# Performance work log

Measured on AMD Instinct MI355X. Metric: run time of the kernel, lower is better.

## Reference

```python
import jax, jax.numpy as jnp
import numpy as np

SEQ, B, V, E, H, L = 64, 64, 32000, 512, 512, 2


def setup_inputs() -> dict:
    key = jax.random.key(0)
    ks = jax.random.split(key, 12)
    k = float(np.sqrt(1.0 / H))
    u = lambda kk, shape, a, b: jax.random.uniform(kk, shape, jnp.float32, a, b)
    return {
        "inputs": jax.random.randint(ks[0], (SEQ, B), 0, V),          # [T, B] token ids
        "hidden": jnp.zeros((L, B, H), jnp.float32),                   # initial hidden
        "emb": u(ks[1], (V, E), -0.1, 0.1),                            # embedding table
        "Wr_w": u(ks[2], (L, H, E + H), -k, k),                        # reset gate [L,H,2H]
        "Wr_b": u(ks[3], (L, H), -k, k),
        "Wz_w": u(ks[4], (L, H, E + H), -k, k),                        # update gate
        "Wz_b": u(ks[5], (L, H), -k, k),
        "Wh_w": u(ks[6], (L, H, E + H), -k, k),                        # candidate
        "Wh_b": u(ks[7], (L, H), -k, k),
        "out_w": u(ks[8], (V, H), -0.1, 0.1),                          # output projection
        "out_b": jnp.zeros((V,), jnp.float32),
    }


def reference(inputs, hidden, emb, Wr_w, Wr_b, Wz_w, Wz_b, Wh_w, Wh_b, out_w, out_b):
    # GRU recurrence over time via lax.scan (dropout disabled: dp_keep_prob=1.0)
    def step(h, tok):
        x = emb[tok]  # [B, E]
        new_h = []
        for i in range(L):  # fixed small layer loop
            hi = h[i]  # [B, H]
            cat = jnp.concatenate([x, hi], axis=1)  # [B, E+H]
            r = jax.nn.sigmoid(cat @ Wr_w[i].T + Wr_b[i])
            z = jax.nn.sigmoid(cat @ Wz_w[i].T + Wz_b[i])
            h_hat = jnp.tanh(jnp.concatenate([x, r * hi], axis=1) @ Wh_w[i].T + Wh_b[i])
            x = (1.0 - z) * hi + z * h_hat  # next layer input / new hidden
            new_h.append(x)
        logits_t = x @ out_w.T + out_b  # [B, V]
        return jnp.stack(new_h), logits_t

    hidden_final, logits = jax.lax.scan(step, hidden, inputs)
    return logits, hidden_final  # [T,B,V], [L,B,H]
```

## Files before the change

### kernel.cpp

```cpp
#include <hip/hip_runtime.h>

constexpr int NT = 64;
constexpr int NB = 64;
constexpr int NV = 32000;
constexpr int NE = 512;
constexpr int NH = 512;
constexpr int NPAIR = 16 * 250;

constexpr size_t SZ_OW  = (size_t)NV * NE;
constexpr size_t SZ_XE  = (size_t)NT * NB * NE;
constexpr size_t SZ_H   = (size_t)NB * NH;
constexpr size_t LOGITS = (size_t)NT * NB * NV;

typedef float f32x4 __attribute__((ext_vector_type(4)));
typedef int   i32x4 __attribute__((ext_vector_type(4)));
typedef short bf16x8 __attribute__((ext_vector_type(8)));
typedef short s16x4 __attribute__((ext_vector_type(4)));
typedef _Float16 f16x8 __attribute__((ext_vector_type(8)));

__device__ __forceinline__ unsigned short f2bf(float x) {
  unsigned u = __float_as_uint(x);
  u += 0x7FFFu + ((u >> 16) & 1u);
  return (unsigned short)(u >> 16);
}
__device__ __forceinline__ float bf2f(unsigned short s) {
  return __uint_as_float(((unsigned)s) << 16);
}
__device__ __forceinline__ void split2(float v, short* hi, short* lo) {
  unsigned short h = f2bf(v);
  *hi = (short)h;
  *lo = (short)f2bf(v - bf2f(h));
}
__device__ __forceinline__ f32x4 mma_bf16(bf16x8 a, bf16x8 b, f32x4 c) {
  return __builtin_amdgcn_mfma_f32_16x16x32_bf16(a, b, c, 0, 0, 0);
}
__device__ __forceinline__ f32x4 mma_f16(f16x8 a, f16x8 b, f32x4 c) {
  return __builtin_amdgcn_mfma_f32_16x16x32_f16(a, b, c, 0, 0, 0);
}
__device__ __forceinline__ float fast_sigmoid(float x) {
  return __builtin_amdgcn_rcpf(1.0f + __expf(-x));
}
__device__ __forceinline__ float fast_tanh(float x) {
  return 1.0f - 2.0f * __builtin_amdgcn_rcpf(1.0f + __expf(2.0f * x));
}

__device__ __forceinline__ void st_sc32u(unsigned* p, unsigned v) {
  asm volatile("global_store_dword %0, %1, off sc0 sc1" :: "v"(p), "v"(v) : "memory");
}
__device__ __forceinline__ void st_sc128(void* p, i32x4 v) {
  asm volatile("global_store_dwordx4 %0, %1, off sc0 sc1" :: "v"(p), "v"(v) : "memory");
}
__device__ __forceinline__ void st_nt(float* p, float v) {
  asm volatile("global_store_dword %0, %1, off nt" :: "v"(p), "v"(v) : "memory");
}
__device__ __forceinline__ unsigned ld_sc32u(const unsigned* p) {
  unsigned v;
  asm volatile("global_load_dword %0, %1, off sc0 sc1\n\ts_waitcnt vmcnt(0)"
               : "=v"(v) : "v"(p) : "memory");
  return v;
}

__device__ __forceinline__ void wait1(const unsigned* flags, int slot, unsigned thr) {
  while (ld_sc32u(&flags[(size_t)slot * 32]) < thr) {}
}
__device__ __forceinline__ void wave_poll4(const unsigned* flags, int slotBase, int cgBase,
                                           int rh, unsigned thr, int lane) {
  const unsigned* fp = &flags[(size_t)(slotBase + (cgBase + (lane & 3)) * 2 + rh) * 32];
  while (!__all((int)(ld_sc32u(fp) >= thr))) {}
}
__device__ __forceinline__ void wave_poll8(const unsigned* flags, int slotBase, int cgBase,
                                           int rh, unsigned thr, int lane) {
  const unsigned* fp = &flags[(size_t)(slotBase + (cgBase + (lane & 7)) * 2 + rh) * 32];
  while (!__all((int)(ld_sc32u(fp) >= thr))) {}
}

__device__ __forceinline__ void publish(unsigned* flags, int slot, unsigned val) {
  asm volatile("s_waitcnt vmcnt(0)" ::: "memory");
  __syncthreads();
  if (threadIdx.x == 0) st_sc32u(&flags[(size_t)slot * 32], val);
}

__global__ void k_prep(
    const float* __restrict__ outw, const int* __restrict__ toks,
    const float* __restrict__ emb, const float* __restrict__ hid,
    _Float16* OWf, short* XeHi, short* XeLo,
    short* X1Hi, short* X1Lo, short* h0Hi, short* h0Lo) {
  const size_t stride = (size_t)gridDim.x * blockDim.x;
  const size_t N1 = SZ_OW, N2 = N1 + SZ_XE, N3 = N2 + SZ_H, N4 = N3 + SZ_H;
  for (size_t x = (size_t)blockIdx.x * blockDim.x + threadIdx.x; x < N4; x += stride) {
    if (x < N1) {
      OWf[x] = (_Float16)outw[x];
    } else if (x < N2) {
      size_t p = x - N1;
      size_t r = p >> 9, c = p & 511u;
      int tok = toks[r];
      float v = emb[(size_t)tok * 512 + c];
      short hi, lo; split2(v, &hi, &lo);
      XeHi[p] = hi; XeLo[p] = lo;
    } else if (x < N3) {
      size_t p = x - N2;
      short hi, lo; split2(hid[p], &hi, &lo);
      h0Hi[p] = hi; h0Lo[p] = lo;
    } else {
      size_t p = x - N3;
      short hi, lo; split2(hid[SZ_H + p], &hi, &lo);
      X1Hi[p] = hi; X1Lo[p] = lo;
    }
  }
}

__device__ __forceinline__ void mmaP32(
    const short* __restrict__ aH, const short* __restrict__ aL, int base,
    const short* lsHi_, const short* lsLo_,
    f32x4 (&accH)[2], f32x4 (&accL)[2], int wave, int l15, int lq) {
  const int kq = wave >> 1, rhalf = wave & 1;
  const int r0 = rhalf * 16 + l15;
#pragma unroll
  for (int i = 0; i < 4; ++i) {
    const int ko = kq * 128 + i * 32 + lq * 8;
    const int kg = base + ko;
    const int e0 = (l15 * 1024 + kg) ^ ((l15 & 7) << 3);
    const int e1 = ((16 + l15) * 1024 + kg) ^ ((l15 & 7) << 3);
    bf16x8 bh0 = *(const bf16x8*)&lsHi_[e0];
    bf16x8 bl0 = *(const bf16x8*)&lsLo_[e0];
    bf16x8 bh1 = *(const bf16x8*)&lsHi_[e1];
    bf16x8 bl1 = *(const bf16x8*)&lsLo_[e1];
    bf16x8 ah = *(const bf16x8*)&aH[r0 * 512 + ko];
    bf16x8 al = *(const bf16x8*)&aL[r0 * 512 + ko];
    accH[0] = mma_bf16(ah, bh0, accH[0]);
    accH[1] = mma_bf16(ah, bh1, accH[1]);
    accL[0] = mma_bf16(al, bh0, accL[0]);
    accL[1] = mma_bf16(al, bh1, accL[1]);
    accL[0] = mma_bf16(ah, bl0, accL[0]);
    accL[1] = mma_bf16(ah, bl1, accL[1]);
  }
}
__device__ __forceinline__ void reduce4(float* lsRed_, f32x4 (&accH)[2], f32x4 (&accL)[2],
                                        f32x4 (&acc)[2], int wave, int l15, int lq) {
  const int kq = wave >> 1, rhalf = wave & 1;
  acc[0] = accH[0] + accL[0];
  acc[1] = accH[1] + accL[1];
  const int pos = l15 * 16 + lq * 4;
  if (kq) {
    *(f32x4*)&lsRed_[(((kq - 1) * 2 + rhalf) * 2 + 0) * 256 + pos] = acc[0];
    *(f32x4*)&lsRed_[(((kq - 1) * 2 + rhalf) * 2 + 1) * 256 + pos] = acc[1];
  }
  __syncthreads();
  if (!kq) {
#pragma unroll
    for (int s = 0; s < 3; ++s) {
      acc[0] += *(const f32x4*)&lsRed_[((s * 2 + rhalf) * 2 + 0) * 256 + pos];
      acc[1] += *(const f32x4*)&lsRed_[((s * 2 + rhalf) * 2 + 1) * 256 + pos];
    }
  }
  __syncthreads();
}

__device__ __forceinline__ void mmaD(
    const short* __restrict__ pAH, const short* __restrict__ pAL,
    int kloc0, int kkGlob0, const short* lsHi_, const short* lsLo_,
    f32x4 (&accH)[2], f32x4 (&accL)[2], int l15, int lq, int rhalf, int rowbase) {
  const int r0 = rowbase + rhalf * 16 + l15;
#pragma unroll 4
  for (int i = 0; i < 8; ++i) {
    const int kk = kkGlob0 + i * 32 + lq * 8;
    const int ka = kloc0 + i * 32 + lq * 8;
    const int e0 = (l15 * 1024 + kk) ^ ((l15 & 7) << 3);
    const int e1 = ((16 + l15) * 1024 + kk) ^ ((l15 & 7) << 3);
    bf16x8 bh0 = *(const bf16x8*)&lsHi_[e0];
    bf16x8 bl0 = *(const bf16x8*)&lsLo_[e0];
    bf16x8 bh1 = *(const bf16x8*)&lsHi_[e1];
    bf16x8 bl1 = *(const bf16x8*)&lsLo_[e1];
    bf16x8 ah = *(const bf16x8*)&pAH[r0 * 512 + ka];
    bf16x8 al = *(const bf16x8*)&pAL[r0 * 512 + ka];
    accH[0] = mma_bf16(ah, bh0, accH[0]);
    accH[1] = mma_bf16(ah, bh1, accH[1]);
    accL[0] = mma_bf16(al, bh0, accL[0]);
    accL[1] = mma_bf16(al, bh1, accL[1]);
    accL[0] = mma_bf16(ah, bl0, accL[0]);
    accL[1] = mma_bf16(ah, bl1, accL[1]);
  }
}
__device__ __forceinline__ void reduceD(float* lsRed_, f32x4 (&accH)[2], f32x4 (&accL)[2],
                                        f32x4 (&acc)[2], int wave, int l15, int lq) {
  acc[0] = accH[0] + accL[0];
  acc[1] = accH[1] + accL[1];
  const int pos = l15 * 16 + lq * 4;
  if (wave >= 2) {
    *(f32x4*)&lsRed_[((wave - 2) * 2 + 0) * 256 + pos] = acc[0];
    *(f32x4*)&lsRed_[((wave - 2) * 2 + 1) * 256 + pos] = acc[1];
  }
  __syncthreads();
  if (wave < 2) {
#pragma unroll
    for (int s = 0; s < 3; ++s) {
      const int slot = (wave & 1) + 2 * s;
      acc[0] += *(const f32x4*)&lsRed_[(slot * 2 + 0) * 256 + pos];
      acc[1] += *(const f32x4*)&lsRed_[(slot * 2 + 1) * 256 + pos];
    }
  }
  __syncthreads();
}

__device__ __forceinline__ void stage_weights(
    short* lsHi, short* lsLo, const float* srcBase0, const float* srcBase1,
    int jc, int tid) {
  for (int i = tid; i < 8192; i += 512) {
    const int j = i >> 8;
    const int k4 = (i & 255) << 2;
    const int g = jc + j;
    const float* src = (srcBase1 && g >= 512)
        ? (srcBase1 + (size_t)(g - 512) * 1024 + k4)
        : (srcBase0 + (size_t)g * 1024 + k4);
    f32x4 v = *(const f32x4*)src;
    s16x4 h4, l4;
#pragma unroll
    for (int q = 0; q < 4; ++q) { short hi, lo; split2(v[q], &hi, &lo); h4[q] = hi; l4[q] = lo; }
    const int els = (j * 1024 + k4) ^ ((j & 7) << 3);
    *(s16x4*)&lsHi[els] = h4;
    *(s16x4*)&lsLo[els] = l4;
  }
}

__device__ void gemm_loop(char* pool, int tid,
                          const _Float16* Af, const _Float16* Bw,
                          const float* bias, float* C,
                          unsigned* flags, unsigned* tcnt) {
  _Float16* lsA0 = (_Float16*)pool;
  _Float16* lsA1 = lsA0 + 128 * 64;
  _Float16* lsB  = lsA1 + 128 * 64;
  volatile int* bc = (volatile int*)(pool + 49152);
  const int wave = tid >> 6, lane = tid & 63, l15 = lane & 15, lq = lane >> 4;
  const int wr = (wave >> 2) * 64, wc = (wave & 3) * 32;
  unsigned lastR = 0;
  __syncthreads();
  for (;;) {
    if (tid == 0)
      *bc = (int)__hip_atomic_fetch_add(tcnt, 1u, __ATOMIC_RELAXED,
                                        __HIP_MEMORY_SCOPE_AGENT);
    __syncthreads();
    const int pr = *bc;
    __syncthreads();
    if (pr >= NPAIR) break;
    const int p = pr / 250, bn = pr - p * 250;
    const unsigned Rneed = 4u * (unsigned)p + 4u;
    if (lastR < Rneed) {
      if (tid < 32) {
        const unsigned* fp = &flags[(size_t)(160 + tid) * 32];
        while (ld_sc32u(fp) < Rneed) __builtin_amdgcn_s_sleep(8);
      }
      lastR = Rneed;
    }
    __syncthreads();
    f32x4 acc0[4][2] = {}, acc1[4][2] = {};
    const size_t arow0 = (size_t)p * 256;
    const size_t brow0 = (size_t)bn * 128;
    for (int kb = 0; kb < 512; kb += 64) {
#pragma unroll
      for (int i = 0; i < 2; ++i) {
        int c = tid + i * 512;
        int row = c >> 3, kc = (c & 7) * 8;
        int el = (row * 64 + kc) ^ ((row & 7) << 3);
        *(f16x8*)&lsA0[el] = *(const f16x8*)(Af + (arow0 + row) * 512 + kb + kc);
        *(f16x8*)&lsA1[el] = *(const f16x8*)(Af + (arow0 + 128 + row) * 512 + kb + kc);
        *(f16x8*)&lsB[el]  = *(const f16x8*)(Bw + (brow0 + row) * 512 + kb + kc);
      }
      __syncthreads();
#pragma unroll
      for (int k0 = 0; k0 < 64; k0 += 32) {
        const int kk = k0 + lq * 8;
        f16x8 af0[4], af1[4], bfr[2];
#pragma unroll
        for (int i = 0; i < 4; ++i) {
          int ra = wr + i * 16 + l15;
          int el = (ra * 64 + kk) ^ ((ra & 7) << 3);
          af0[i] = *(const f16x8*)&lsA0[el];
          af1[i] = *(const f16x8*)&lsA1[el];
        }
#pragma unroll
        for (int jt = 0; jt < 2; ++jt) {
          int rb = wc + jt * 16 + l15;
          bfr[jt] = *(const f16x8*)&lsB[(rb * 64 + kk) ^ ((rb & 7) << 3)];
        }
#pragma unroll
        for (int i = 0; i < 4; ++i)
#pragma unroll
          for (int jt = 0; jt < 2; ++jt) {
            acc0[i][jt] = mma_f16(af0[i], bfr[jt], acc0[i][jt]);
            acc1[i][jt] = mma_f16(af1[i], bfr[jt], acc1[i][jt]);
          }
      }
      __syncthreads();
    }
    const float b0v = bias[brow0 + wc + l15];
    const float b1v = bias[brow0 + wc + 16 + l15];
#pragma unroll
    for (int i = 0; i < 4; ++i) {
#pragma unroll
      for (int r = 0; r < 4; ++r) {
        const size_t row = arow0 + wr + i * 16 + lq * 4 + r;
        float* pa = C + row * (size_t)NV + brow0 + wc + l15;
        st_nt(pa, acc0[i][0][r] + b0v);
        st_nt(pa + 16, acc0[i][1][r] + b1v);
        float* pb = pa + (size_t)128 * NV;
        st_nt(pb, acc1[i][0][r] + b0v);
        st_nt(pb + 16, acc1[i][1][r] + b1v);
      }
    }
  }
}

__launch_bounds__(512, 1)
__global__ void k_main(
    const float* __restrict__ Wr, const float* __restrict__ Wz, const float* __restrict__ Wh,
    const float* __restrict__ Wrb, const float* __restrict__ Wzb, const float* __restrict__ Whb,
    const short* __restrict__ XeHi, const short* __restrict__ XeLo,
    short* X1Hi, short* X1Lo, _Float16* X1f16,
    short* h0Hi, short* h0Lo,
    short* rh0Hi, short* rh0Lo, short* rh1Hi, short* rh1Lo,
    float* z0, float* z1, float* hidOut,
    const _Float16* OWf, const float* outb, float* out,
    unsigned* flags, unsigned* tcnt) {
  __shared__ __align__(16) char pool[153600];
  short* lsHi = (short*)pool;
  short* lsLo = lsHi + 32 * 1024;
  float* lsRed = (float*)(pool + 131072);
  short* sH    = (short*)(pool + 131072);
  short* sL    = sH + 1024;
  float* sZA   = (float*)(pool + 131072);
  short* stH   = (short*)(pool + 143360);
  short* stL   = stH + 1024;
  float* sZ    = (float*)(pool + 147456);
  _Float16* sX = (_Float16*)(pool + 151552);

  const int wg = blockIdx.x;
  const int tid = threadIdx.x;
  const int wave = tid >> 6, lane = tid & 63, l15 = lane & 15, lq = lane >> 4;

  if (wg < 64) {
    const int cg = wg >> 1, rh = wg & 1, jc = cg * 32, rowbase = rh * 32;
    const bool isR = (jc < 512);
    stage_weights(lsHi, lsLo, Wr, Wz, jc, tid);
    float biasL0, biasL1;
    {
      const int j0 = jc + l15, j1 = j0 + 16;
      biasL0 = (j0 < 512) ? Wrb[j0] : Wzb[j0 - 512];
      biasL1 = (j1 < 512) ? Wrb[j1] : Wzb[j1 - 512];
    }
    __syncthreads();
    for (int t = 0; t < NT; ++t) {
      f32x4 accH[2] = {}, accL[2] = {};
      mmaP32(XeHi + (size_t)t * SZ_H + rowbase * 512,
             XeLo + (size_t)t * SZ_H + rowbase * 512, 0,
             lsHi, lsLo, accH, accL, wave, l15, lq);
      const short* hH = h0Hi + (size_t)t * SZ_H + rowbase * 512;
      const short* hL = h0Lo + (size_t)t * SZ_H + rowbase * 512;
      i32x4 pre;
      const int pbuf = tid >> 7, pq = tid & 127, prow = pq >> 2, pc = pq & 3;
      if (isR && tid < 256) {
        wait1(flags, 128 + ((jc >> 5) * 2 + rh), (unsigned)t);
        pre = *(const i32x4*)((pbuf ? hL : hH) + prow * 512 + jc + pc * 8);
      }
      wave_poll4(flags, 128, 4 * (wave >> 1), rh, (unsigned)t, lane);
      mmaP32(hH, hL, 512, lsHi, lsLo, accH, accL, wave, l15, lq);
      if (isR && tid < 256)
        *(i32x4*)&(pbuf ? stL : stH)[prow * 32 + pc * 8] = pre;
      f32x4 acc[2];
      reduce4(lsRed, accH, accL, acc, wave, l15, lq);
      if (wave < 2) {
#pragma unroll
        for (int ct = 0; ct < 2; ++ct) {
          const int jj = ct * 16 + l15;
          const float bv = ct ? biasL1 : biasL0;
#pragma unroll
          for (int r = 0; r < 4; ++r) {
            const int lb = wave * 16 + lq * 4 + r;
            const float s = fast_sigmoid(acc[ct][r] + bv);
            if (isR) {
              const float hv = bf2f((unsigned short)stH[lb * 32 + jj]) +
                               bf2f((unsigned short)stL[lb * 32 + jj]);
              short hi, lo; split2(s * hv, &hi, &lo);
              sH[lb * 32 + jj] = hi; sL[lb * 32 + jj] = lo;
            } else {
              sZA[lb * 32 + jj] = s;
            }
          }
        }
      }
      __syncthreads();
      if (isR) {
        if (tid < 256) {
          i32x4 v = *(const i32x4*)&(pbuf ? sL : sH)[prow * 32 + pc * 8];
          st_sc128((pbuf ? rh0Lo : rh0Hi) + (size_t)t * SZ_H +
                   (size_t)(rowbase + prow) * 512 + jc + pc * 8, v);
        }
      } else {
        if (tid < 256) {
          const int row = tid >> 3, c = tid & 7;
          i32x4 v = *(const i32x4*)&sZA[row * 32 + c * 4];
          st_sc128(z0 + (size_t)t * SZ_H + (size_t)(rowbase + row) * 512 +
                   (jc - 512) + c * 4, v);
        }
      }
      publish(flags, wg, (unsigned)(t + 1));
    }
  } else if (wg < 128) {
    const int idx = wg - 64, cg = idx >> 1, rh = idx & 1, jc = cg * 32, rowbase = rh * 32;
    const bool isR = (jc < 512);
    stage_weights(lsHi, lsLo, Wr + (size_t)512 * 1024, Wz + (size_t)512 * 1024, jc, tid);
    float biasL0, biasL1;
    {
      const int j0 = jc + l15, j1 = j0 + 16;
      biasL0 = (j0 < 512) ? Wrb[512 + j0] : Wzb[512 + j0 - 512];
      biasL1 = (j1 < 512) ? Wrb[512 + j1] : Wzb[512 + j1 - 512];
    }
    __syncthreads();
    for (int t = 0; t < NT; ++t) {
      const short* xH = h0Hi + (size_t)(t + 1) * SZ_H;
      const short* xL = h0Lo + (size_t)(t + 1) * SZ_H;
      const short* hH = X1Hi + (size_t)t * SZ_H;
      const short* hL = X1Lo + (size_t)t * SZ_H;
      i32x4 pre;
      const int pbuf = tid >> 7, pq = tid & 127, prow = pq >> 2, pc = pq & 3;
      if (isR && tid < 256) {
        wait1(flags, 160 + ((jc >> 5) * 2 + rh), (unsigned)t);
        pre = *(const i32x4*)((pbuf ? hL : hH) +
                              (size_t)(rowbase + prow) * 512 + jc + pc * 8);
      }
      f32x4 accH[2] = {}, accL[2] = {};
      {
        const int khalf = wave >> 1, rhalf = wave & 1;
        if (khalf < 2) wave_poll8(flags, 128, (khalf & 1) * 8, rh, (unsigned)(t + 1), lane);
        else           wave_poll8(flags, 160, (khalf & 1) * 8, rh, (unsigned)t, lane);
        const short* pAH = (khalf < 2) ? xH : hH;
        const short* pAL = (khalf < 2) ? xL : hL;
        mmaD(pAH, pAL, (khalf & 1) * 256, khalf * 256, lsHi, lsLo,
             accH, accL, l15, lq, rhalf, rowbase);
      }
      if (isR && tid < 256)
        *(i32x4*)&(pbuf ? stL : stH)[prow * 32 + pc * 8] = pre;
      f32x4 acc[2];
      reduceD(lsRed, accH, accL, acc, wave, l15, lq);
      if (wave < 2) {
#pragma unroll
        for (int ct = 0; ct < 2; ++ct) {
          const int jj = ct * 16 + l15;
          const float bv = ct ? biasL1 : biasL0;
#pragma unroll
          for (int r = 0; r < 4; ++r) {
            const int lb = wave * 16 + lq * 4 + r;
            const float s = fast_sigmoid(acc[ct][r] + bv);
            if (isR) {
              const float hv = bf2f((unsigned short)stH[lb * 32 + jj]) +
                               bf2f((unsigned short)stL[lb * 32 + jj]);
              short hi, lo; split2(s * hv, &hi, &lo);
              sH[lb * 32 + jj] = hi; sL[lb * 32 + jj] = lo;
            } else {
              sZA[lb * 32 + jj] = s;
            }
          }
        }
      }
      __syncthreads();
      if (isR) {
        if (tid < 256) {
          i32x4 v = *(const i32x4*)&(pbuf ? sL : sH)[prow * 32 + pc * 8];
          st_sc128((pbuf ? rh1Lo : rh1Hi) + (size_t)t * SZ_H +
                   (size_t)(rowbase + prow) * 512 + jc + pc * 8, v);
        }
      } else {
        if (tid < 256) {
          const int row = tid >> 3, c = tid & 7;
          i32x4 v = *(const i32x4*)&sZA[row * 32 + c * 4];
          st_sc128(z1 + (size_t)t * SZ_H + (size_t)(rowbase + row) * 512 +
                   (jc - 512) + c * 4, v);
        }
      }
      publish(flags, wg, (unsigned)(t + 1));
    }
  } else if (wg < 192) {
    const bool isL1 = (wg >= 160);
    const int idx = isL1 ? (wg - 160) : (wg - 128);
    const int cg = idx >> 1, rh = idx & 1, jc = cg * 32, rowbase = rh * 32;
    const int layer = isL1 ? 1 : 0;
    stage_weights(lsHi, lsLo, Wh + (size_t)layer * 512 * 1024, nullptr, jc, tid);
    const float biasL0 = Whb[layer * 512 + jc + l15];
    const float biasL1 = Whb[layer * 512 + jc + 16 + l15];
    __syncthreads();
    short* myHi = isL1 ? X1Hi : h0Hi;
    short* myLo = isL1 ? X1Lo : h0Lo;
    const short* rhHi_ = isL1 ? rh1Hi : rh0Hi;
    const short* rhLo_ = isL1 ? rh1Lo : rh0Lo;
    const float* zArr = isL1 ? z1 : z0;
    const int fbase = isL1 ? 64 : 0;
    for (int t = 0; t < NT; ++t) {
      const int pbuf = tid >> 7, pq = tid & 127, prow = pq >> 2, pc = pq & 3;
      if (tid < 256) {
        const short* src = (pbuf ? myLo : myHi) + (size_t)t * SZ_H +
                           (size_t)(rowbase + prow) * 512 + jc + pc * 8;
        *(i32x4*)&(pbuf ? stL : stH)[prow * 32 + pc * 8] = *(const i32x4*)src;
      }
      f32x4 accH[2] = {}, accL[2] = {};
      if (isL1) {
        wave_poll4(flags, 128, 4 * (wave >> 1), rh, (unsigned)(t + 1), lane);
        mmaP32(h0Hi + (size_t)(t + 1) * SZ_H + rowbase * 512,
               h0Lo + (size_t)(t + 1) * SZ_H + rowbase * 512, 0,
               lsHi, lsLo, accH, accL, wave, l15, lq);
      } else {
        mmaP32(XeHi + (size_t)t * SZ_H + rowbase * 512,
               XeLo + (size_t)t * SZ_H + rowbase * 512, 0,
               lsHi, lsLo, accH, accL, wave, l15, lq);
      }
      f32x4 zv;
      const int zrow = tid >> 3, zc = tid & 7;
      if (tid < 256) {
        wait1(flags, fbase + ((16 + (jc >> 5)) * 2 + rh), (unsigned)(t + 1));
        zv = *(const f32x4*)(zArr + (size_t)t * SZ_H +
                             (size_t)(rowbase + zrow) * 512 + jc + zc * 4);
      }
      wave_poll4(flags, fbase, 4 * (wave >> 1), rh, (unsigned)(t + 1), lane);
      mmaP32(rhHi_ + (size_t)t * SZ_H + rowbase * 512,
             rhLo_ + (size_t)t * SZ_H + rowbase * 512, 512,
             lsHi, lsLo, accH, accL, wave, l15, lq);
      if (tid < 256)
        *(f32x4*)&sZ[zrow * 32 + zc * 4] = zv;
      f32x4 acc[2];
      reduce4(lsRed, accH, accL, acc, wave, l15, lq);
      if (wave < 2) {
#pragma unroll
        for (int ct = 0; ct < 2; ++ct) {
          const int jj = ct * 16 + l15, j = jc + jj;
          const float bv = ct ? biasL1 : biasL0;
#pragma unroll
          for (int r = 0; r < 4; ++r) {
            const int lb = wave * 16 + lq * 4 + r;
            const float hh = fast_tanh(acc[ct][r] + bv);
            const float z = sZ[lb * 32 + jj];
            const float ho = bf2f((unsigned short)stH[lb * 32 + jj]) +
                             bf2f((unsigned short)stL[lb * 32 + jj]);
            const float hn = (1.0f - z) * ho + z * hh;
            short hi, lo; split2(hn, &hi, &lo);
            sH[lb * 32 + jj] = hi; sL[lb * 32 + jj] = lo;
            if (isL1) sX[lb * 32 + jj] = (_Float16)hn;
            if (t == NT - 1)
              hidOut[(size_t)layer * SZ_H + (size_t)(rowbase + lb) * 512 + j] = hn;
          }
        }
      }
      __syncthreads();
      if (tid < 256) {
        i32x4 v = *(const i32x4*)&(pbuf ? sL : sH)[prow * 32 + pc * 8];
        st_sc128((pbuf ? myLo : myHi) + (size_t)(t + 1) * SZ_H +
                 (size_t)(rowbase + prow) * 512 + jc + pc * 8, v);
      } else if (isL1 && tid < 384) {
        const int q = tid - 256, row = q >> 2, c = q & 3;
        i32x4 v = *(const i32x4*)&sX[row * 32 + c * 8];
        st_sc128(X1f16 + (size_t)t * SZ_H + (size_t)(rowbase + row) * 512 + jc + c * 8, v);
      }
      publish(flags, wg, (unsigned)(t + 1));
    }
  }
  gemm_loop(pool, tid, X1f16, OWf, outb, out, flags, tcnt);
}

extern "C" void kernel_launch(void* const* d_in, const int* in_sizes, int n_in,
                              void* d_out, int out_size, void* d_ws, size_t ws_size,
                              hipStream_t stream) {
  (void)in_sizes; (void)n_in; (void)out_size; (void)ws_size;
  const int*   toks = (const int*)d_in[0];
  const float* hid  = (const float*)d_in[1];
  const float* emb  = (const float*)d_in[2];
  const float* Wr   = (const float*)d_in[3];
  const float* Wrb  = (const float*)d_in[4];
  const float* Wz   = (const float*)d_in[5];
  const float* Wzb  = (const float*)d_in[6];
  const float* Wh   = (const float*)d_in[7];
  const float* Whb  = (const float*)d_in[8];
  const float* outw = (const float*)d_in[9];
  const float* outb = (const float*)d_in[10];
  float* out = (float*)d_out;

  char* base = (char*)d_ws;
  size_t off = 0;
  auto carve = [&](size_t bytes) -> char* {
    char* r = base + off;
    off = (off + bytes + 255) & ~(size_t)255;
    return r;
  };
  _Float16* OWf   = (_Float16*)carve(SZ_OW * 2);
  short*    XeHi  = (short*)carve(SZ_XE * 2);
  short*    XeLo  = (short*)carve(SZ_XE * 2);
  short*    X1Hi  = (short*)carve((size_t)(NT + 1) * SZ_H * 2);
  short*    X1Lo  = (short*)carve((size_t)(NT + 1) * SZ_H * 2);
  _Float16* X1f16 = (_Float16*)carve((size_t)NT * SZ_H * 2);
  short*    h0Hi  = (short*)carve((size_t)(NT + 1) * SZ_H * 2);
  short*    h0Lo  = (short*)carve((size_t)(NT + 1) * SZ_H * 2);
  short*    rh0Hi = (short*)carve((size_t)NT * SZ_H * 2);
  short*    rh0Lo = (short*)carve((size_t)NT * SZ_H * 2);
  short*    rh1Hi = (short*)carve((size_t)NT * SZ_H * 2);
  short*    rh1Lo = (short*)carve((size_t)NT * SZ_H * 2);
  float*    z0    = (float*)carve((size_t)NT * SZ_H * 4);
  float*    z1    = (float*)carve((size_t)NT * SZ_H * 4);
  unsigned* flags = (unsigned*)carve(32768);
  unsigned* tcnt  = (unsigned*)carve(256);

  hipMemsetAsync(flags, 0, 32768, stream);
  hipMemsetAsync(tcnt, 0, 256, stream);

  k_prep<<<2048, 256, 0, stream>>>(outw, toks, emb, hid,
                                   OWf, XeHi, XeLo, X1Hi, X1Lo, h0Hi, h0Lo);

  k_main<<<256, 512, 0, stream>>>(
      Wr, Wz, Wh, Wrb, Wzb, Whb, XeHi, XeLo,
      X1Hi, X1Lo, X1f16, h0Hi, h0Lo,
      rh0Hi, rh0Lo, rh1Hi, rh1Lo, z0, z1,
      out + LOGITS, OWf, outb, out, flags, tcnt);
}
```

Baseline: 698.4 us.

## Switch GRU recurrence to per-wave tiles with wave-level flags and no block barriers

Reorganizes the persistent recurrent workgroups so each wave computes a full 16x16 output tile over the whole K range, removing cross-wave LDS reductions and __syncthreads. Synchronization moves from per-workgroup flags to per-wave flags, so consumers poll only the specific producer tiles they need. The recurrent workgroup count drops from 192 to 96 (each handles all 64 batch rows), and the hidden state stays in registers instead of being reloaded. The aim is a shorter serial critical path per timestep, at the cost of more flag polling traffic and more K-work per wave.

Result: slower. 1.668 ms (+138.8%).

```diff
diff --git a/kernel.cpp b/kernel.cpp
--- a/kernel.cpp
+++ b/kernel.cpp
@@ -60,24 +60,12 @@
   return v;
 }
 
-__device__ __forceinline__ void wait1(const unsigned* flags, int slot, unsigned thr) {
-  while (ld_sc32u(&flags[(size_t)slot * 32]) < thr) {}
-}
-__device__ __forceinline__ void wave_poll4(const unsigned* flags, int slotBase, int cgBase,
-                                           int rh, unsigned thr, int lane) {
-  const unsigned* fp = &flags[(size_t)(slotBase + (cgBase + (lane & 3)) * 2 + rh) * 32];
+__device__ __forceinline__ void wave_poll(const unsigned* fp, unsigned thr) {
   while (!__all((int)(ld_sc32u(fp) >= thr))) {}
 }
-__device__ __forceinline__ void wave_poll8(const unsigned* flags, int slotBase, int cgBase,
-                                           int rh, unsigned thr, int lane) {
-  const unsigned* fp = &flags[(size_t)(slotBase + (cgBase + (lane & 7)) * 2 + rh) * 32];
-  while (!__all((int)(ld_sc32u(fp) >= thr))) {}
-}
-
-__device__ __forceinline__ void publish(unsigned* flags, int slot, unsigned val) {
+__device__ __forceinline__ void wpublish(unsigned* flags, int slot, unsigned val, int lane) {
   asm volatile("s_waitcnt vmcnt(0)" ::: "memory");
-  __syncthreads();
-  if (threadIdx.x == 0) st_sc32u(&flags[(size_t)slot * 32], val);
+  if (lane == 0) st_sc32u(&flags[(size_t)slot * 32], val);
 }
 
 __global__ void k_prep(
@@ -109,97 +97,31 @@
   }
 }
 
-__device__ __forceinline__ void mmaP32(
-    const short* __restrict__ aH, const short* __restrict__ aL, int base,
-    const short* lsHi_, const short* lsLo_,
-    f32x4 (&accH)[2], f32x4 (&accL)[2], int wave, int l15, int lq) {
-  const int kq = wave >> 1, rhalf = wave & 1;
-  const int r0 = rhalf * 16 + l15;
-#pragma unroll
-  for (int i = 0; i < 4; ++i) {
-    const int ko = kq * 128 + i * 32 + lq * 8;
-    const int kg = base + ko;
-    const int e0 = (l15 * 1024 + kg) ^ ((l15 & 7) << 3);
-    const int e1 = ((16 + l15) * 1024 + kg) ^ ((l15 & 7) << 3);
-    bf16x8 bh0 = *(const bf16x8*)&lsHi_[e0];
-    bf16x8 bl0 = *(const bf16x8*)&lsLo_[e0];
-    bf16x8 bh1 = *(const bf16x8*)&lsHi_[e1];
-    bf16x8 bl1 = *(const bf16x8*)&lsLo_[e1];
-    bf16x8 ah = *(const bf16x8*)&aH[r0 * 512 + ko];
-    bf16x8 al = *(const bf16x8*)&aL[r0 * 512 + ko];
-    accH[0] = mma_bf16(ah, bh0, accH[0]);
-    accH[1] = mma_bf16(ah, bh1, accH[1]);
-    accL[0] = mma_bf16(al, bh0, accL[0]);
-    accL[1] = mma_bf16(al, bh1, accL[1]);
-    accL[0] = mma_bf16(ah, bl0, accL[0]);
-    accL[1] = mma_bf16(ah, bl1, accL[1]);
+__device__ __forceinline__ void waveMMA16(
+    const short* __restrict__ aH, const short* __restrict__ aL,
+    int r0, int wkb, const short* lsHi_, const short* lsLo_, int wrow,
+    f32x4 (&accH)[2], f32x4 (&accL)[2], int lq) {
+#pragma unroll
+  for (int blk = 0; blk < 16; blk += 8) {
+    bf16x8 ah[8], al[8];
+#pragma unroll
+    for (int i = 0; i < 8; ++i) {
+      const int ka = (blk + i) * 32 + lq * 8;
+      ah[i] = *(const bf16x8*)&aH[r0 * 512 + ka];
+      al[i] = *(const bf16x8*)&aL[r0 * 512 + ka];
+    }
+#pragma unroll
+    for (int i = 0; i < 8; ++i) {
+      const int kg = wkb + (blk + i) * 32 + lq * 8;
+      const int e = (wrow * 1024 + kg) ^ ((wrow & 7) << 3);
+      bf16x8 bh = *(const bf16x8*)&lsHi_[e];
+      bf16x8 bl = *(const bf16x8*)&lsLo_[e];
+      const int p = i & 1;
+      accH[p] = mma_bf16(ah[i], bh, accH[p]);
+      accL[p] = mma_bf16(al[i], bh, accL[p]);
+      accL[p] = mma_bf16(ah[i], bl, accL[p]);
+    }
   }
-}
-__device__ __forceinline__ void reduce4(float* lsRed_, f32x4 (&accH)[2], f32x4 (&accL)[2],
-                                        f32x4 (&acc)[2], int wave, int l15, int lq) {
-  const int kq = wave >> 1, rhalf = wave & 1;
-  acc[0] = accH[0] + accL[0];
-  acc[1] = accH[1] + accL[1];
-  const int pos = l15 * 16 + lq * 4;
-  if (kq) {
-    *(f32x4*)&lsRed_[(((kq - 1) * 2 + rhalf) * 2 + 0) * 256 + pos] = acc[0];
-    *(f32x4*)&lsRed_[(((kq - 1) * 2 + rhalf) * 2 + 1) * 256 + pos] = acc[1];
-  }
-  __syncthreads();
-  if (!kq) {
-#pragma unroll
-    for (int s = 0; s < 3; ++s) {
-      acc[0] += *(const f32x4*)&lsRed_[((s * 2 + rhalf) * 2 + 0) * 256 + pos];
-      acc[1] += *(const f32x4*)&lsRed_[((s * 2 + rhalf) * 2 + 1) * 256 + pos];
-    }
-  }
-  __syncthreads();
-}
-
-__device__ __forceinline__ void mmaD(
-    const short* __restrict__ pAH, const short* __restrict__ pAL,
-    int kloc0, int kkGlob0, const short* lsHi_, const short* lsLo_,
-    f32x4 (&accH)[2], f32x4 (&accL)[2], int l15, int lq, int rhalf, int rowbase) {
-  const int r0 = rowbase + rhalf * 16 + l15;
-#pragma unroll 4
-  for (int i = 0; i < 8; ++i) {
-    const int kk = kkGlob0 + i * 32 + lq * 8;
-    const int ka = kloc0 + i * 32 + lq * 8;
-    const int e0 = (l15 * 1024 + kk) ^ ((l15 & 7) << 3);
-    const int e1 = ((16 + l15) * 1024 + kk) ^ ((l15 & 7) << 3);
-    bf16x8 bh0 = *(const bf16x8*)&lsHi_[e0];
-    bf16x8 bl0 = *(const bf16x8*)&lsLo_[e0];
-    bf16x8 bh1 = *(const bf16x8*)&lsHi_[e1];
-    bf16x8 bl1 = *(const bf16x8*)&lsLo_[e1];
-    bf16x8 ah = *(const bf16x8*)&pAH[r0 * 512 + ka];
-    bf16x8 al = *(const bf16x8*)&pAL[r0 * 512 + ka];
-    accH[0] = mma_bf16(ah, bh0, accH[0]);
-    accH[1] = mma_bf16(ah, bh1, accH[1]);
-    accL[0] = mma_bf16(al, bh0, accL[0]);
-    accL[1] = mma_bf16(al, bh1, accL[1]);
-    accL[0] = mma_bf16(ah, bl0, accL[0]);
-    accL[1] = mma_bf16(ah, bl1, accL[1]);
-  }
-}
-__device__ __forceinline__ void reduceD(float* lsRed_, f32x4 (&accH)[2], f32x4 (&accL)[2],
-                                        f32x4 (&acc)[2], int wave, int l15, int lq) {
-  acc[0] = accH[0] + accL[0];
-  acc[1] = accH[1] + accL[1];
-  const int pos = l15 * 16 + lq * 4;
-  if (wave >= 2) {
-    *(f32x4*)&lsRed_[((wave - 2) * 2 + 0) * 256 + pos] = acc[0];
-    *(f32x4*)&lsRed_[((wave - 2) * 2 + 1) * 256 + pos] = acc[1];
-  }
-  __syncthreads();
-  if (wave < 2) {
-#pragma unroll
-    for (int s = 0; s < 3; ++s) {
-      const int slot = (wave & 1) + 2 * s;
-      acc[0] += *(const f32x4*)&lsRed_[(slot * 2 + 0) * 256 + pos];
-      acc[1] += *(const f32x4*)&lsRed_[(slot * 2 + 1) * 256 + pos];
-    }
-  }
-  __syncthreads();
 }
 
 __device__ __forceinline__ void stage_weights(
@@ -220,6 +142,18 @@
     *(s16x4*)&lsHi[els] = h4;
     *(s16x4*)&lsLo[els] = l4;
   }
+}
+
+__device__ __forceinline__ void wave_store16(
+    const short* scrH, const short* scrL,
+    short* gHi, short* gLo, int rt, int colBase, int lane) {
+  asm volatile("s_waitcnt lgkmcnt(0)" ::: "memory");
+  const int rr = lane >> 2, cc = lane & 3;
+  i32x4 v;
+  if (cc < 2) v = *(const i32x4*)&scrH[rr * 16 + cc * 8];
+  else        v = *(const i32x4*)&scrL[rr * 16 + (cc - 2) * 8];
+  short* dst = (cc < 2 ? gHi : gLo) + (size_t)(rt * 16 + rr) * 512 + colBase + (cc & 1) * 8;
+  st_sc128(dst, v);
 }
 
 __device__ void gemm_loop(char* pool, int tid,
@@ -245,9 +179,13 @@
     const int p = pr / 250, bn = pr - p * 250;
     const unsigned Rneed = 4u * (unsigned)p + 4u;
     if (lastR < Rneed) {
-      if (tid < 32) {
-        const unsigned* fp = &flags[(size_t)(160 + tid) * 32];
-        while (ld_sc32u(fp) < Rneed) __builtin_amdgcn_s_sleep(8);
+      {
+        const unsigned* fp = &flags[(size_t)((80 + (lane >> 3)) * 8 + (lane & 7)) * 32];
+        while (!__all((int)(ld_sc32u(fp) >= Rneed))) __builtin_amdgcn_s_sleep(8);
+      }
+      {
+        const unsigned* fp = &flags[(size_t)((88 + (lane >> 3)) * 8 + (lane & 7)) * 32];
+        while (!__all((int)(ld_sc32u(fp) >= Rneed))) __builtin_amdgcn_s_sleep(8);
       }
       lastR = Rneed;
     }
@@ -314,6 +252,7 @@
 __global__ void k_main(
     const float* __restrict__ Wr, const float* __restrict__ Wz, const float* __restrict__ Wh,
     const float* __restrict__ Wrb, const float* __restrict__ Wzb, const float* __restrict__ Whb,
+    const float* __restrict__ hid,
     const short* __restrict__ XeHi, const short* __restrict__ XeLo,
     short* X1Hi, short* X1Lo, _Float16* X1f16,
     short* h0Hi, short* h0Lo,
@@ -321,243 +260,194 @@
     float* z0, float* z1, float* hidOut,
     const _Float16* OWf, const float* outb, float* out,
     unsigned* flags, unsigned* tcnt) {
-  __shared__ __align__(16) char pool[153600];
+  __shared__ __align__(16) char pool[147456];
   short* lsHi = (short*)pool;
   short* lsLo = lsHi + 32 * 1024;
-  float* lsRed = (float*)(pool + 131072);
-  short* sH    = (short*)(pool + 131072);
-  short* sL    = sH + 1024;
-  float* sZA   = (float*)(pool + 131072);
-  short* stH   = (short*)(pool + 143360);
-  short* stL   = stH + 1024;
-  float* sZ    = (float*)(pool + 147456);
-  _Float16* sX = (_Float16*)(pool + 151552);
+  char* wscrBase = pool + 131072;
 
   const int wg = blockIdx.x;
   const int tid = threadIdx.x;
   const int wave = tid >> 6, lane = tid & 63, l15 = lane & 15, lq = lane >> 4;
+  const int ct = wave >> 2, rt = wave & 3;
+  const int r0 = rt * 16 + l15;
+  short* scrH = (short*)(wscrBase + wave * 2048);
+  short* scrL = scrH + 256;
+  _Float16* scrX = (_Float16*)(scrH + 512);
+  float* scrF = (float*)scrH;
 
   if (wg < 64) {
-    const int cg = wg >> 1, rh = wg & 1, jc = cg * 32, rowbase = rh * 32;
-    const bool isR = (jc < 512);
-    stage_weights(lsHi, lsLo, Wr, Wz, jc, tid);
-    float biasL0, biasL1;
+    const bool isL1 = (wg >= 32);
+    const int cg = isL1 ? (wg - 32) : wg;
+    const int jc = cg * 32;
+    const bool isR = (cg < 16);
+    const int wrow = ct * 16 + l15;
+    stage_weights(lsHi, lsLo, Wr + (isL1 ? (size_t)512 * 1024 : 0),
+                  Wz + (isL1 ? (size_t)512 * 1024 : 0), jc, tid);
+    float bv;
     {
-      const int j0 = jc + l15, j1 = j0 + 16;
-      biasL0 = (j0 < 512) ? Wrb[j0] : Wzb[j0 - 512];
-      biasL1 = (j1 < 512) ? Wrb[j1] : Wzb[j1 - 512];
-    }
+      const int j = jc + ct * 16 + l15;
+      bv = (j < 512) ? Wrb[(isL1 ? 512 : 0) + j] : Wzb[(isL1 ? 512 : 0) + j - 512];
+    }
+    short* outHi = isL1 ? rh1Hi : rh0Hi;
+    short* outLo = isL1 ? rh1Lo : rh0Lo;
+    float* outZ  = isL1 ? z1 : z0;
     __syncthreads();
     for (int t = 0; t < NT; ++t) {
       f32x4 accH[2] = {}, accL[2] = {};
-      mmaP32(XeHi + (size_t)t * SZ_H + rowbase * 512,
-             XeLo + (size_t)t * SZ_H + rowbase * 512, 0,
-             lsHi, lsLo, accH, accL, wave, l15, lq);
-      const short* hH = h0Hi + (size_t)t * SZ_H + rowbase * 512;
-      const short* hL = h0Lo + (size_t)t * SZ_H + rowbase * 512;
-      i32x4 pre;
-      const int pbuf = tid >> 7, pq = tid & 127, prow = pq >> 2, pc = pq & 3;
-      if (isR && tid < 256) {
-        wait1(flags, 128 + ((jc >> 5) * 2 + rh), (unsigned)t);
-        pre = *(const i32x4*)((pbuf ? hL : hH) + prow * 512 + jc + pc * 8);
-      }
-      wave_poll4(flags, 128, 4 * (wave >> 1), rh, (unsigned)t, lane);
-      mmaP32(hH, hL, 512, lsHi, lsLo, accH, accL, wave, l15, lq);
-      if (isR && tid < 256)
-        *(i32x4*)&(pbuf ? stL : stH)[prow * 32 + pc * 8] = pre;
-      f32x4 acc[2];
-      reduce4(lsRed, accH, accL, acc, wave, l15, lq);
-      if (wave < 2) {
-#pragma unroll
-        for (int ct = 0; ct < 2; ++ct) {
-          const int jj = ct * 16 + l15;
-          const float bv = ct ? biasL1 : biasL0;
-#pragma unroll
-          for (int r = 0; r < 4; ++r) {
-            const int lb = wave * 16 + lq * 4 + r;
-            const float s = fast_sigmoid(acc[ct][r] + bv);
-            if (isR) {
-              const float hv = bf2f((unsigned short)stH[lb * 32 + jj]) +
-                               bf2f((unsigned short)stL[lb * 32 + jj]);
-              short hi, lo; split2(s * hv, &hi, &lo);
-              sH[lb * 32 + jj] = hi; sL[lb * 32 + jj] = lo;
-            } else {
-              sZA[lb * 32 + jj] = s;
-            }
+      const short *hH, *hL;
+      if (!isL1) {
+        waveMMA16(XeHi + (size_t)t * SZ_H, XeLo + (size_t)t * SZ_H,
+                  r0, 0, lsHi, lsLo, wrow, accH, accL, lq);
+        {
+          const unsigned* fp; unsigned thr;
+          if (lane < 32) {
+            const int bb = lane >> 1, ctp = lane & 1;
+            fp = &flags[(size_t)((64 + bb) * 8 + ctp * 4 + rt) * 32]; thr = (unsigned)t;
+          } else { fp = flags; thr = 0u; }
+          wave_poll(fp, thr);
+        }
+        hH = h0Hi + (size_t)t * SZ_H; hL = h0Lo + (size_t)t * SZ_H;
+      } else {
+        {
+          const unsigned* fp; unsigned thr;
+          if (lane < 32) {
+            const int bb = lane >> 1, ctp = lane & 1;
+            fp = &flags[(size_t)((64 + bb) * 8 + ctp * 4 + rt) * 32]; thr = (unsigned)(t + 1);
+          } else {
+            const int li = lane - 32, bb = li >> 1, ctp = li & 1;
+            fp = &flags[(size_t)((80 + bb) * 8 + ctp * 4 + rt) * 32]; thr = (unsigned)t;
           }
-        }
-      }
-      __syncthreads();
+          wave_poll(fp, thr);
+        }
+        hH = X1Hi + (size_t)t * SZ_H; hL = X1Lo + (size_t)t * SZ_H;
+      }
+      float hv[4];
       if (isR) {
-        if (tid < 256) {
-          i32x4 v = *(const i32x4*)&(pbuf ? sL : sH)[prow * 32 + pc * 8];
-          st_sc128((pbuf ? rh0Lo : rh0Hi) + (size_t)t * SZ_H +
-                   (size_t)(rowbase + prow) * 512 + jc + pc * 8, v);
-        }
+#pragma unroll
+        for (int r = 0; r < 4; ++r) {
+          const int row = rt * 16 + lq * 4 + r, col = jc + ct * 16 + l15;
+          hv[r] = bf2f((unsigned short)hH[row * 512 + col]) +
+                  bf2f((unsigned short)hL[row * 512 + col]);
+        }
+      }
+      if (!isL1) {
+        waveMMA16(hH, hL, r0, 512, lsHi, lsLo, wrow, accH, accL, lq);
       } else {
-        if (tid < 256) {
-          const int row = tid >> 3, c = tid & 7;
-          i32x4 v = *(const i32x4*)&sZA[row * 32 + c * 4];
-          st_sc128(z0 + (size_t)t * SZ_H + (size_t)(rowbase + row) * 512 +
-                   (jc - 512) + c * 4, v);
-        }
-      }
-      publish(flags, wg, (unsigned)(t + 1));
-    }
-  } else if (wg < 128) {
-    const int idx = wg - 64, cg = idx >> 1, rh = idx & 1, jc = cg * 32, rowbase = rh * 32;
-    const bool isR = (jc < 512);
-    stage_weights(lsHi, lsLo, Wr + (size_t)512 * 1024, Wz + (size_t)512 * 1024, jc, tid);
-    float biasL0, biasL1;
-    {
-      const int j0 = jc + l15, j1 = j0 + 16;
-      biasL0 = (j0 < 512) ? Wrb[512 + j0] : Wzb[512 + j0 - 512];
-      biasL1 = (j1 < 512) ? Wrb[512 + j1] : Wzb[512 + j1 - 512];
-    }
-    __syncthreads();
-    for (int t = 0; t < NT; ++t) {
-      const short* xH = h0Hi + (size_t)(t + 1) * SZ_H;
-      const short* xL = h0Lo + (size_t)(t + 1) * SZ_H;
-      const short* hH = X1Hi + (size_t)t * SZ_H;
-      const short* hL = X1Lo + (size_t)t * SZ_H;
-      i32x4 pre;
-      const int pbuf = tid >> 7, pq = tid & 127, prow = pq >> 2, pc = pq & 3;
-      if (isR && tid < 256) {
-        wait1(flags, 160 + ((jc >> 5) * 2 + rh), (unsigned)t);
-        pre = *(const i32x4*)((pbuf ? hL : hH) +
-                              (size_t)(rowbase + prow) * 512 + jc + pc * 8);
-      }
-      f32x4 accH[2] = {}, accL[2] = {};
-      {
-        const int khalf = wave >> 1, rhalf = wave & 1;
-        if (khalf < 2) wave_poll8(flags, 128, (khalf & 1) * 8, rh, (unsigned)(t + 1), lane);
-        else           wave_poll8(flags, 160, (khalf & 1) * 8, rh, (unsigned)t, lane);
-        const short* pAH = (khalf < 2) ? xH : hH;
-        const short* pAL = (khalf < 2) ? xL : hL;
-        mmaD(pAH, pAL, (khalf & 1) * 256, khalf * 256, lsHi, lsLo,
-             accH, accL, l15, lq, rhalf, rowbase);
-      }
-      if (isR && tid < 256)
-        *(i32x4*)&(pbuf ? stL : stH)[prow * 32 + pc * 8] = pre;
-      f32x4 acc[2];
-      reduceD(lsRed, accH, accL, acc, wave, l15, lq);
-      if (wave < 2) {
-#pragma unroll
-        for (int ct = 0; ct < 2; ++ct) {
-          const int jj = ct * 16 + l15;
-          const float bv = ct ? biasL1 : biasL0;
-#pragma unroll
-          for (int r = 0; r < 4; ++r) {
-            const int lb = wave * 16 + lq * 4 + r;
-            const float s = fast_sigmoid(acc[ct][r] + bv);
-            if (isR) {
-              const float hv = bf2f((unsigned short)stH[lb * 32 + jj]) +
-                               bf2f((unsigned short)stL[lb * 32 + jj]);
-              short hi, lo; split2(s * hv, &hi, &lo);
-              sH[lb * 32 + jj] = hi; sL[lb * 32 + jj] = lo;
-            } else {
-              sZA[lb * 32 + jj] = s;
-            }
-          }
-        }
-      }
-      __syncthreads();
+        waveMMA16(h0Hi + (size_t)(t + 1) * SZ_H, h0Lo + (size_t)(t + 1) * SZ_H,
+                  r0, 0, lsHi, lsLo, wrow, accH, accL, lq);
+        waveMMA16(hH, hL, r0, 512, lsHi, lsLo, wrow, accH, accL, lq);
+      }
+      f32x4 acc = accH[0] + accH[1] + accL[0] + accL[1];
       if (isR) {
-        if (tid < 256) {
-          i32x4 v = *(const i32x4*)&(pbuf ? sL : sH)[prow * 32 + pc * 8];
-          st_sc128((pbuf ? rh1Lo : rh1Hi) + (size_t)t * SZ_H +
-                   (size_t)(rowbase + prow) * 512 + jc + pc * 8, v);
-        }
+#pragma unroll
+        for (int r = 0; r < 4; ++r) {
+          const float s = fast_sigmoid(acc[r] + bv);
+          short hi, lo; split2(s * hv[r], &hi, &lo);
+          scrH[(lq * 4 + r) * 16 + l15] = hi;
+          scrL[(lq * 4 + r) * 16 + l15] = lo;
+        }
+        wave_store16(scrH, scrL, outHi + (size_t)t * SZ_H, outLo + (size_t)t * SZ_H,
+                     rt, jc + ct * 16, lane);
       } else {
-        if (tid < 256) {
-          const int row = tid >> 3, c = tid & 7;
-          i32x4 v = *(const i32x4*)&sZA[row * 32 + c * 4];
-          st_sc128(z1 + (size_t)t * SZ_H + (size_t)(rowbase + row) * 512 +
-                   (jc - 512) + c * 4, v);
-        }
-      }
-      publish(flags, wg, (unsigned)(t + 1));
-    }
-  } else if (wg < 192) {
-    const bool isL1 = (wg >= 160);
-    const int idx = isL1 ? (wg - 160) : (wg - 128);
-    const int cg = idx >> 1, rh = idx & 1, jc = cg * 32, rowbase = rh * 32;
+#pragma unroll
+        for (int r = 0; r < 4; ++r)
+          scrF[(lq * 4 + r) * 16 + l15] = fast_sigmoid(acc[r] + bv);
+        asm volatile("s_waitcnt lgkmcnt(0)" ::: "memory");
+        const int rr = lane >> 2, cc = lane & 3;
+        f32x4 v = *(const f32x4*)&scrF[rr * 16 + cc * 4];
+        st_sc128(outZ + (size_t)t * SZ_H + (size_t)(rt * 16 + rr) * 512 +
+                 (jc - 512) + ct * 16 + cc * 4, __builtin_bit_cast(i32x4, v));
+      }
+      wpublish(flags, wg * 8 + wave, (unsigned)(t + 1), lane);
+    }
+  } else if (wg < 96) {
+    const bool isL1 = (wg >= 80);
+    const int b = isL1 ? (wg - 80) : (wg - 64);
+    const int jc = b * 32;
     const int layer = isL1 ? 1 : 0;
+    const int wrow = ct * 16 + l15;
     stage_weights(lsHi, lsLo, Wh + (size_t)layer * 512 * 1024, nullptr, jc, tid);
-    const float biasL0 = Whb[layer * 512 + jc + l15];
-    const float biasL1 = Whb[layer * 512 + jc + 16 + l15];
-    __syncthreads();
+    const float bv = Whb[layer * 512 + jc + ct * 16 + l15];
+    f32x4 hOld;
+#pragma unroll
+    for (int r = 0; r < 4; ++r)
+      hOld[r] = hid[(size_t)layer * SZ_H + (size_t)(rt * 16 + lq * 4 + r) * 512 +
+                    jc + ct * 16 + l15];
     short* myHi = isL1 ? X1Hi : h0Hi;
     short* myLo = isL1 ? X1Lo : h0Lo;
     const short* rhHi_ = isL1 ? rh1Hi : rh0Hi;
     const short* rhLo_ = isL1 ? rh1Lo : rh0Lo;
     const float* zArr = isL1 ? z1 : z0;
-    const int fbase = isL1 ? 64 : 0;
+    __syncthreads();
     for (int t = 0; t < NT; ++t) {
-      const int pbuf = tid >> 7, pq = tid & 127, prow = pq >> 2, pc = pq & 3;
-      if (tid < 256) {
-        const short* src = (pbuf ? myLo : myHi) + (size_t)t * SZ_H +
-                           (size_t)(rowbase + prow) * 512 + jc + pc * 8;
-        *(i32x4*)&(pbuf ? stL : stH)[prow * 32 + pc * 8] = *(const i32x4*)src;
-      }
       f32x4 accH[2] = {}, accL[2] = {};
-      if (isL1) {
-        wave_poll4(flags, 128, 4 * (wave >> 1), rh, (unsigned)(t + 1), lane);
-        mmaP32(h0Hi + (size_t)(t + 1) * SZ_H + rowbase * 512,
-               h0Lo + (size_t)(t + 1) * SZ_H + rowbase * 512, 0,
-               lsHi, lsLo, accH, accL, wave, l15, lq);
+      if (!isL1) {
+        waveMMA16(XeHi + (size_t)t * SZ_H, XeLo + (size_t)t * SZ_H,
+                  r0, 0, lsHi, lsLo, wrow, accH, accL, lq);
+        {
+          const unsigned* fp; unsigned thr = (unsigned)(t + 1);
+          if (lane < 32) {
+            const int cgp = lane >> 1, ctp = lane & 1;
+            fp = &flags[(size_t)(cgp * 8 + ctp * 4 + rt) * 32];
+          } else if (lane == 32) {
+            fp = &flags[(size_t)((16 + b) * 8 + ct * 4 + rt) * 32];
+          } else { fp = flags; thr = 0u; }
+          wave_poll(fp, thr);
+        }
       } else {
-        mmaP32(XeHi + (size_t)t * SZ_H + rowbase * 512,
-               XeLo + (size_t)t * SZ_H + rowbase * 512, 0,
-               lsHi, lsLo, accH, accL, wave, l15, lq);
-      }
-      f32x4 zv;
-      const int zrow = tid >> 3, zc = tid & 7;
-      if (tid < 256) {
-        wait1(flags, fbase + ((16 + (jc >> 5)) * 2 + rh), (unsigned)(t + 1));
-        zv = *(const f32x4*)(zArr + (size_t)t * SZ_H +
-                             (size_t)(rowbase + zrow) * 512 + jc + zc * 4);
-      }
-      wave_poll4(flags, fbase, 4 * (wave >> 1), rh, (unsigned)(t + 1), lane);
-      mmaP32(rhHi_ + (size_t)t * SZ_H + rowbase * 512,
-             rhLo_ + (size_t)t * SZ_H + rowbase * 512, 512,
-             lsHi, lsLo, accH, accL, wave, l15, lq);
-      if (tid < 256)
-        *(f32x4*)&sZ[zrow * 32 + zc * 4] = zv;
-      f32x4 acc[2];
-      reduce4(lsRed, accH, accL, acc, wave, l15, lq);
-      if (wave < 2) {
-#pragma unroll
-        for (int ct = 0; ct < 2; ++ct) {
-          const int jj = ct * 16 + l15, j = jc + jj;
-          const float bv = ct ? biasL1 : biasL0;
-#pragma unroll
-          for (int r = 0; r < 4; ++r) {
-            const int lb = wave * 16 + lq * 4 + r;
-            const float hh = fast_tanh(acc[ct][r] + bv);
-            const float z = sZ[lb * 32 + jj];
-            const float ho = bf2f((unsigned short)stH[lb * 32 + jj]) +
-                             bf2f((unsigned short)stL[lb * 32 + jj]);
-            const float hn = (1.0f - z) * ho + z * hh;
-            short hi, lo; split2(hn, &hi, &lo);
-            sH[lb * 32 + jj] = hi; sL[lb * 32 + jj] = lo;
-            if (isL1) sX[lb * 32 + jj] = (_Float16)hn;
-            if (t == NT - 1)
-              hidOut[(size_t)layer * SZ_H + (size_t)(rowbase + lb) * 512 + j] = hn;
-          }
-        }
-      }
-      __syncthreads();
-      if (tid < 256) {
-        i32x4 v = *(const i32x4*)&(pbuf ? sL : sH)[prow * 32 + pc * 8];
-        st_sc128((pbuf ? myLo : myHi) + (size_t)(t + 1) * SZ_H +
-                 (size_t)(rowbase + prow) * 512 + jc + pc * 8, v);
-      } else if (isL1 && tid < 384) {
-        const int q = tid - 256, row = q >> 2, c = q & 3;
-        i32x4 v = *(const i32x4*)&sX[row * 32 + c * 8];
-        st_sc128(X1f16 + (size_t)t * SZ_H + (size_t)(rowbase + row) * 512 + jc + c * 8, v);
-      }
-      publish(flags, wg, (unsigned)(t + 1));
+        {
+          const unsigned* fp; unsigned thr;
+          if (lane < 32) {
+            const int bb = lane >> 1, ctp = lane & 1;
+            fp = &flags[(size_t)((64 + bb) * 8 + ctp * 4 + rt) * 32]; thr = (unsigned)(t + 1);
+          } else { fp = flags; thr = 0u; }
+          wave_poll(fp, thr);
+        }
+        waveMMA16(h0Hi + (size_t)(t + 1) * SZ_H, h0Lo + (size_t)(t + 1) * SZ_H,
+                  r0, 0, lsHi, lsLo, wrow, accH, accL, lq);
+        {
+          const unsigned* fp; unsigned thr = (unsigned)(t + 1);
+          if (lane < 32) {
+            const int cgp = lane >> 1, ctp = lane & 1;
+            fp = &flags[(size_t)((32 + cgp) * 8 + ctp * 4 + rt) * 32];
+          } else if (lane == 32) {
+            fp = &flags[(size_t)((48 + b) * 8 + ct * 4 + rt) * 32];
+          } else { fp = flags; thr = 0u; }
+          wave_poll(fp, thr);
+        }
+      }
+      float zv[4];
+#pragma unroll
+      for (int r = 0; r < 4; ++r)
+        zv[r] = zArr[(size_t)t * SZ_H + (size_t)(rt * 16 + lq * 4 + r) * 512 +
+                     jc + ct * 16 + l15];
+      waveMMA16(rhHi_ + (size_t)t * SZ_H, rhLo_ + (size_t)t * SZ_H,
+                r0, 512, lsHi, lsLo, wrow, accH, accL, lq);
+      f32x4 acc = accH[0] + accH[1] + accL[0] + accL[1];
+      f32x4 hnew;
+#pragma unroll
+      for (int r = 0; r < 4; ++r) {
+        const float hh = fast_tanh(acc[r] + bv);
+        const float hn = (1.0f - zv[r]) * hOld[r] + zv[r] * hh;
+        hnew[r] = hn;
+        short hi, lo; split2(hn, &hi, &lo);
+        scrH[(lq * 4 + r) * 16 + l15] = hi;
+        scrL[(lq * 4 + r) * 16 + l15] = lo;
+        if (isL1) scrX[(lq * 4 + r) * 16 + l15] = (_Float16)hn;
+        if (t == NT - 1)
+          hidOut[(size_t)layer * SZ_H + (size_t)(rt * 16 + lq * 4 + r) * 512 +
+                 jc + ct * 16 + l15] = hn;
+      }
+      hOld = hnew;
+      wave_store16(scrH, scrL, myHi + (size_t)(t + 1) * SZ_H, myLo + (size_t)(t + 1) * SZ_H,
+                   rt, jc + ct * 16, lane);
+      if (isL1 && lane < 32) {
+        const int rr = lane >> 1, cc = lane & 1;
+        i32x4 v = *(const i32x4*)&scrX[rr * 16 + cc * 8];
+        st_sc128(X1f16 + (size_t)t * SZ_H + (size_t)(rt * 16 + rr) * 512 +
+                 jc + ct * 16 + cc * 8, v);
+      }
+      wpublish(flags, wg * 8 + wave, (unsigned)(t + 1), lane);
     }
   }
   gemm_loop(pool, tid, X1f16, OWf, outb, out, flags, tcnt);
@@ -601,17 +491,17 @@
   short*    rh1Lo = (short*)carve((size_t)NT * SZ_H * 2);
   float*    z0    = (float*)carve((size_t)NT * SZ_H * 4);
   float*    z1    = (float*)carve((size_t)NT * SZ_H * 4);
-  unsigned* flags = (unsigned*)carve(32768);
+  unsigned* flags = (unsigned*)carve(98304);
   unsigned* tcnt  = (unsigned*)carve(256);
 
-  hipMemsetAsync(flags, 0, 32768, stream);
+  hipMemsetAsync(flags, 0, 98304, stream);
   hipMemsetAsync(tcnt, 0, 256, stream);
 
   k_prep<<<2048, 256, 0, stream>>>(outw, toks, emb, hid,
                                    OWf, XeHi, XeLo, X1Hi, X1Lo, h0Hi, h0Lo);
 
   k_main<<<256, 512, 0, stream>>>(
-      Wr, Wz, Wh, Wrb, Wzb, Whb, XeHi, XeLo,
+      Wr, Wz, Wh, Wrb, Wzb, Whb, hid, XeHi, XeLo,
       X1Hi, X1Lo, X1f16, h0Hi, h0Lo,
       rh0Hi, rh0Lo, rh1Hi, rh1Lo, z0, z1,
       out + LOGITS, OWf, outb, out, flags, tcnt);
```
